# Kernel tuning notes

Measured on AMD Instinct MI355X. Metric: run time of the kernel, lower is better.

The kernel has to match this reference:

```python
import jax, jax.numpy as jnp
import numpy as np
from jax import lax

HD = 64      # head_dim
PS = 2       # fine patch size
EPS = 1e-5   # batchnorm eps

def _conv(x, w, stride, pad, groups=1):
    return lax.conv_general_dilated(x, w, (stride, stride), ((pad, pad), (pad, pad)),
                                    feature_group_count=groups,
                                    dimension_numbers=('NCHW', 'OIHW', 'NCHW'))

def _conv_transpose(x, w, stride, pad):
    # torch ConvTranspose2d(in,out,k,stride,pad) with w [in,out,k,k]
    k = w.shape[-1]
    wt = jnp.flip(w, (2, 3)).transpose(1, 0, 2, 3)  # -> [out,in,k,k]
    e = k - 1 - pad
    return lax.conv_general_dilated(x, wt, (1, 1), ((e, e), (e, e)),
                                    lhs_dilation=(stride, stride),
                                    dimension_numbers=('NCHW', 'OIHW', 'NCHW'))

def _bn(x, g, b, m, v):
    inv = g / jnp.sqrt(v + EPS)
    return x * inv[None, :, None, None] + (b - m * inv)[None, :, None, None]

def setup_inputs() -> dict:
    key = jax.random.key(0)
    ks = jax.random.split(key, 12)
    B, C, H, W = 8, 256, 64, 64
    f = lambda k, sh, s=0.05: jax.random.normal(k, sh, jnp.float32) * s
    return {
        'x': jax.random.normal(ks[0], (B, C, H, W), jnp.float32),
        'down_w': f(ks[1], (C, C, 4, 4), 0.02), 'down_b': f(ks[2], (C,)),
        'up_w': f(ks[3], (C, C, 4, 4), 0.02), 'up_b': f(ks[4], (C,)),
        'wqkv_c': f(ks[5], (HD, 3 * HD)), 'bqkv_c': f(ks[6], (3 * HD,)),
        'wqkv_f': f(ks[7], (HD, 3 * HD)), 'bqkv_f': f(ks[8], (3 * HD,)),
        'dw_w': f(ks[9], (C, 1, 3, 3)),
        'bn1_g': jnp.ones((C,), jnp.float32), 'bn1_b': jnp.zeros((C,), jnp.float32),
        'bn1_m': jnp.zeros((C,), jnp.float32), 'bn1_v': jnp.ones((C,), jnp.float32),
        'pw_w': f(ks[10], (C, C, 1, 1)),
        'bn2_g': jnp.ones((C,), jnp.float32), 'bn2_b': jnp.zeros((C,), jnp.float32),
        'bn2_m': jnp.zeros((C,), jnp.float32), 'bn2_v': jnp.ones((C,), jnp.float32),
    }

def reference(x, down_w, down_b, up_w, up_b, wqkv_c, bqkv_c, wqkv_f, bqkv_f, dw_w,
              bn1_g, bn1_b, bn1_m, bn1_v, pw_w, bn2_g, bn2_b, bn2_m, bn2_v):
    B, C, H, W = x.shape
    nh = C // HD
    scale = HD ** -0.5

    # ---- CoarseSelfAttention: downsample -> per-head MHSA -> top-k -> upsample ----
    xd = _conv(x, down_w, 2, 1) + down_b[None, :, None, None]          # [B,C,H/2,W/2]
    h, w = H // 2, W // 2
    N = h * w
    tok = xd.reshape(B, nh, HD, N).transpose(0, 1, 3, 2)               # [B,nh,N,hd]
    q, k, v = jnp.split(tok @ wqkv_c + bqkv_c, 3, axis=-1)
    attn = jax.nn.softmax(jnp.einsum('bhnd,bhmd->bhnm', q, k) * scale, axis=-1)
    score = attn.sum(axis=-2)                                          # [B,nh,N]
    kf = max(1, N // 4)
    topk = lax.top_k(score, kf)[1]                                     # [B,nh,kf] int32
    out = jnp.einsum('bhnm,bhmd->bhnd', attn, v)
    out = out.transpose(0, 1, 3, 2).reshape(B, C, h, w)
    coarse = _conv_transpose(out, up_w, 2, 1) + up_b[None, :, None, None]  # [B,C,H,W]
    # F.interpolate to (H,W) is identity here: upsample output already matches x.

    # ---- TopkSelfAttention: gather top-k 2x2 patches, local MHSA, scatter back ----
    ph, pw = H // PS, W // PS
    xh = coarse.reshape(B, nh, HD, ph, PS, pw, PS)
    patches = xh.transpose(0, 1, 2, 3, 5, 4, 6).reshape(B, nh, HD, ph * pw, PS, PS)
    sel = jnp.take_along_axis(patches, topk[:, :, None, :, None, None], axis=3)  # [B,nh,hd,kf,PS,PS]
    tok_f = sel.reshape(B, nh, HD, kf, PS * PS).transpose(0, 1, 3, 4, 2).reshape(B, nh, kf * PS * PS, HD)
    qf, kfp, vf = jnp.split(tok_f @ wqkv_f + bqkv_f, 3, axis=-1)
    attn_f = jax.nn.softmax(jnp.einsum('bhnd,bhmd->bhnm', qf, kfp) * scale, axis=-1)
    out_f = jnp.einsum('bhnm,bhmd->bhnd', attn_f, vf)                  # [B,nh,kf*4,hd]
    out_p = out_f.reshape(B, nh, kf, PS * PS, HD).transpose(0, 1, 2, 4, 3).reshape(B, nh, kf, HD, PS, PS)
    bi = jnp.arange(B)[:, None, None]
    hi = jnp.arange(nh)[None, :, None]
    res = jnp.zeros_like(patches).at[bi, hi, :, topk].set(out_p)       # scatter (indices unique)
    region = res.reshape(B, nh, HD, ph, pw, PS, PS).transpose(0, 1, 2, 3, 5, 4, 6).reshape(B, C, H, W)

    # ---- residual + DWConv (depthwise->BN->ReLU6->pointwise->BN->ReLU6) ----
    y = coarse + region
    y = jnp.clip(_bn(_conv(y, dw_w, 1, 1, groups=C), bn1_g, bn1_b, bn1_m, bn1_v), 0.0, 6.0)
    y = jnp.clip(_bn(_conv(y, pw_w, 1, 0), bn2_g, bn2_b, bn2_m, bn2_v), 0.0, 6.0)
    return y
```

## Files before the change

kernel.cpp:

```cpp
#include <hip/hip_runtime.h>
#include <hip/hip_bf16.h>

typedef __hip_bfloat16 bf16;
typedef __bf16 bf16x8 __attribute__((ext_vector_type(8)));
typedef float f32x4 __attribute__((ext_vector_type(4)));


#define OFF_XDHWC    0L
#define OFF_QH       2097152L
#define OFF_T1       0L
#define OFF_OUTC     8388608L
#define OFF_COARSE   10485760L
#define OFF_XHL      10485760L
#define OFF_PSCW     10485760L
#define OFF_SCORE    19398656L
#define OFF_TOPK     19431424L
#define OFF_DOWNW    19439616L
#define OFF_DOWNWL   19963904L
#define OFF_UPW4     20488192L
#define OFF_WQKVC    21536768L
#define OFF_BQKVC    21549056L
#define OFF_WQKVF    21549248L
#define OFF_BQKVF    21561536L
#define OFF_PWW      21561728L
#define OFF_DWW      21627264L
#define OFF_BN1S     21629568L
#define OFF_BN1T     21629824L
#define OFF_BN2S     21630080L
#define OFF_BN2T     21630336L
#define OFF_DOWNB    21630592L
#define OFF_UPB      21630848L
#define OFF_FLAG     21631104L
#define WS_FLOATS    21631360L

__device__ __forceinline__ float relu6(float v) { return v < 0.f ? 0.f : (v > 6.f ? 6.f : v); }

__device__ __forceinline__ float ldin(const void* p, long i, int flag) {
    return flag ? __bfloat162float(((const bf16*)p)[i]) : ((const float*)p)[i];
}

__device__ __forceinline__ unsigned short f2bf(float f) {
    unsigned int b = __float_as_uint(f);
    b += 0x7FFFu + ((b >> 16) & 1u);
    return (unsigned short)(b >> 16);
}

__global__ __launch_bounds__(256) void detect_kernel(const void* __restrict__ x, int* __restrict__ flag) {
    __shared__ int cnt[256];
    int tid = threadIdx.x;
    int c = 0;
    for (int i = tid; i < 4096; i += 256) {
        long idx = (long)i * 2047;
        float v = __bfloat162float(((const bf16*)x)[idx]);
        float a = fabsf(v);
        if (isfinite(v) && a > 1e-8f && a < 100.f) c++;
    }
    cnt[tid] = c; __syncthreads();
    for (int s = 128; s > 0; s >>= 1) { if (tid < s) cnt[tid] += cnt[tid + s]; __syncthreads(); }
    if (tid == 0 && cnt[0] >= 3686) *flag = 1;
}

__global__ __launch_bounds__(256) void split_pack_kernel(const void* __restrict__ in, unsigned int* __restrict__ out,
                                                         int n, const int* __restrict__ flagp) {
    int flag = *flagp;
    int i = blockIdx.x * 256 + threadIdx.x;
    if (i < n) {
        float v = ldin(in, i, flag);
        unsigned short h = f2bf(v);
        float fh = __uint_as_float(((unsigned int)h) << 16);
        unsigned short l = f2bf(v - fh);
        out[i] = (unsigned int)h | ((unsigned int)l << 16);
    }
}

__global__ __launch_bounds__(256) void split_kernel(const void* __restrict__ in,
                                                    unsigned short* __restrict__ hi, unsigned short* __restrict__ lo,
                                                    int n, const int* __restrict__ flagp) {
    int flag = *flagp;
    int i = blockIdx.x * 256 + threadIdx.x;
    if (i < n) {
        float v = ldin(in, i, flag);
        unsigned short h = f2bf(v);
        float fh = __uint_as_float(((unsigned int)h) << 16);
        hi[i] = h;
        lo[i] = f2bf(v - fh);
    }
}

__global__ __launch_bounds__(256) void prep_up_kernel(const void* __restrict__ w, unsigned short* __restrict__ W4,
                                                      const int* __restrict__ flagp) {
    int flag = *flagp;
    int idx = blockIdx.x * 256 + threadIdx.x;
    int cls = idx >> 18; int rem = idx & 262143;
    int co = rem >> 10; int q = rem & 1023;
    int ci = q >> 2; int j = q & 3;
    int pa = cls >> 1, pb = cls & 1;
    int jy = j >> 1, jx = j & 1;
    int ky = (pa == 0) ? (jy ? 3 : 1) : (jy ? 0 : 2);
    int kx = (pb == 0) ? (jx ? 3 : 1) : (jx ? 0 : 2);
    W4[idx] = f2bf(ldin(w, (((long)ci * 256 + co) * 4 + ky) * 4 + kx, flag));
}

__global__ __launch_bounds__(256) void prep_misc_kernel(
    const void* __restrict__ down_b, const void* __restrict__ up_b,
    const void* __restrict__ bqkv_c, const void* __restrict__ bqkv_f,
    const void* __restrict__ dw_w, const void* __restrict__ wqkv_c,
    const void* __restrict__ wqkv_f, const void* __restrict__ pw_w,
    const void* __restrict__ bn1_g, const void* __restrict__ bn1_b,
    const void* __restrict__ bn1_m, const void* __restrict__ bn1_v,
    const void* __restrict__ bn2_g, const void* __restrict__ bn2_b,
    const void* __restrict__ bn2_m, const void* __restrict__ bn2_v,
    float* __restrict__ ws, const int* __restrict__ flagp)
{
    int flag = *flagp;
    int bid = blockIdx.x, tid = threadIdx.x;
    if (bid < 48) {
        int idx = bid * 256 + tid;
        int j = idx >> 6, d = idx & 63;
        ws[OFF_WQKVC + idx] = ldin(wqkv_c, d * 192 + j, flag);
    } else if (bid < 96) {
        int idx = (bid - 48) * 256 + tid;
        int j = idx >> 6, d = idx & 63;
        ws[OFF_WQKVF + idx] = ldin(wqkv_f, d * 192 + j, flag);
    } else if (bid < 105) {
        int i = (bid - 96) * 256 + tid;
        if (i < 2304) ws[OFF_DWW + i] = ldin(dw_w, i, flag);
    } else if (bid == 105) {
        ws[OFF_DOWNB + tid] = ldin(down_b, tid, flag);
    } else if (bid == 106) {
        ws[OFF_UPB + tid] = ldin(up_b, tid, flag);
    } else if (bid == 107) {
        if (tid < 192) ws[OFF_BQKVC + tid] = ldin(bqkv_c, tid, flag);
    } else if (bid == 108) {
        if (tid < 192) ws[OFF_BQKVF + tid] = ldin(bqkv_f, tid, flag);
    } else if (bid == 109) {
        float gv = ldin(bn1_g, tid, flag), bv = ldin(bn1_b, tid, flag);
        float mv = ldin(bn1_m, tid, flag), vv = ldin(bn1_v, tid, flag);
        float inv = gv / sqrtf(vv + 1e-5f);
        ws[OFF_BN1S + tid] = inv; ws[OFF_BN1T + tid] = bv - mv * inv;
    } else if (bid == 110) {
        float gv = ldin(bn2_g, tid, flag), bv = ldin(bn2_b, tid, flag);
        float mv = ldin(bn2_m, tid, flag), vv = ldin(bn2_v, tid, flag);
        float inv = gv / sqrtf(vv + 1e-5f);
        ws[OFF_BN2S + tid] = inv; ws[OFF_BN2T + tid] = bv - mv * inv;
    } else {
        int i = (bid - 111) * 256 + tid;
        ((unsigned short*)(ws + OFF_PWW))[i] = f2bf(ldin(pw_w, i, flag));
    }
}

__global__ __launch_bounds__(256) void gemm_mfma_x2(
    const unsigned int* __restrict__ XHL,
    const unsigned short* __restrict__ WH, const unsigned short* __restrict__ WL,
    float* __restrict__ C, const float* __restrict__ e0)
{
    __shared__ __align__(16) unsigned short Ah[64 * 40];
    __shared__ __align__(16) unsigned short Al[64 * 40];
    __shared__ __align__(16) unsigned short Bh[32 * 40];
    __shared__ __align__(16) unsigned short Bl[32 * 40];
    int m0 = blockIdx.y * 64, n0 = blockIdx.x * 32;
    int tid = threadIdx.x;
    int w = tid >> 6, l = tid & 63, l15 = l & 15, q = l >> 4;

    int offA[8], ldsA[8];
    #pragma unroll
    for (int i = 0; i < 8; i++) {
        int idx = i * 256 + tid;
        int kl = idx & 31, ml = idx >> 5;
        int m = m0 + ml;
        int b = m >> 10, oy = (m >> 5) & 31, ox = m & 31;
        int c0 = kl >> 4;
        int ky = (kl >> 2) & 3, kx = kl & 3;
        int iy = 2 * oy - 1 + ky, ix = 2 * ox - 1 + kx;
        ldsA[i] = ml * 40 + kl;
        offA[i] = ((unsigned)iy < 64u && (unsigned)ix < 64u)
                  ? (((b * 256 + c0) * 64 + iy) * 64 + ix) : -1;
    }
    unsigned int aR[8];
    uint2 bhR, blR;
    int bn = tid >> 3, bk = (tid & 7) * 4;

    auto loadA = [&](int k0) {
        int cb = (k0 >> 4) * 4096;
        #pragma unroll
        for (int i = 0; i < 8; i++)
            aR[i] = (offA[i] >= 0) ? XHL[offA[i] + cb] : 0u;
    };
    auto storeA = [&]() {
        #pragma unroll
        for (int i = 0; i < 8; i++) {
            Ah[ldsA[i]] = (unsigned short)(aR[i] & 0xffffu);
            Al[ldsA[i]] = (unsigned short)(aR[i] >> 16);
        }
    };
    auto loadB = [&](int k0) {
        bhR = *(const uint2*)(WH + (long)(n0 + bn) * 4096 + (k0 + bk));
        blR = *(const uint2*)(WL + (long)(n0 + bn) * 4096 + (k0 + bk));
    };

    f32x4 acc[2] = {};
    loadA(0); loadB(0);
    for (int k0 = 0; k0 < 4096; k0 += 32) {
        storeA();
        *(uint2*)(&Bh[bn * 40 + bk]) = bhR;
        *(uint2*)(&Bl[bn * 40 + bk]) = blR;
        __syncthreads();
        if (k0 + 32 < 4096) { loadA(k0 + 32); loadB(k0 + 32); }
        bf16x8 afh = *(const bf16x8*)(&Ah[(w * 16 + l15) * 40 + q * 8]);
        bf16x8 afl = *(const bf16x8*)(&Al[(w * 16 + l15) * 40 + q * 8]);
        #pragma unroll
        for (int j4 = 0; j4 < 2; j4++) {
            bf16x8 bfh = *(const bf16x8*)(&Bh[(j4 * 16 + l15) * 40 + q * 8]);
            bf16x8 bfl = *(const bf16x8*)(&Bl[(j4 * 16 + l15) * 40 + q * 8]);
            acc[j4] = __builtin_amdgcn_mfma_f32_16x16x32_bf16(afh, bfh, acc[j4], 0, 0, 0);
            acc[j4] = __builtin_amdgcn_mfma_f32_16x16x32_bf16(afh, bfl, acc[j4], 0, 0, 0);
            acc[j4] = __builtin_amdgcn_mfma_f32_16x16x32_bf16(afl, bfh, acc[j4], 0, 0, 0);
        }
        __syncthreads();
    }
    #pragma unroll
    for (int j4 = 0; j4 < 2; j4++) {
        int n = n0 + j4 * 16 + l15;
        #pragma unroll
        for (int r = 0; r < 4; r++) {
            int m = m0 + w * 16 + q * 4 + r;
            C[(long)m * 256 + n] = acc[j4][r] + e0[n];
        }
    }
}

template<int EPI>
__global__ __launch_bounds__(256) void gemm_k(
    const float* __restrict__ A, const float* __restrict__ B,
    unsigned short* __restrict__ out, int K, int sAm, int sBn, const float* __restrict__ e0)
{
    __shared__ float As[16][68];
    __shared__ float Bs[16][68];
    int m0 = blockIdx.y * 64;
    int n0 = blockIdx.x * 64;
    int tid = threadIdx.x;
    int tx = tid & 15, ty = tid >> 4;
    int l4 = tid >> 2, kq = (tid & 3) * 4;
    float4 aR, bR;

    auto loadA = [&](int k0) { aR = *(const float4*)(A + (long)(m0 + l4) * sAm + (k0 + kq)); };
    auto loadB = [&](int k0) { bR = *(const float4*)(B + (long)(n0 + l4) * sBn + (k0 + kq)); };

    float acc[4][4] = {};
    loadA(0); loadB(0);
    for (int k0 = 0; k0 < K; k0 += 16) {
        As[kq + 0][l4] = aR.x; As[kq + 1][l4] = aR.y; As[kq + 2][l4] = aR.z; As[kq + 3][l4] = aR.w;
        Bs[kq + 0][l4] = bR.x; Bs[kq + 1][l4] = bR.y; Bs[kq + 2][l4] = bR.z; Bs[kq + 3][l4] = bR.w;
        __syncthreads();
        if (k0 + 16 < K) { loadA(k0 + 16); loadB(k0 + 16); }
        #pragma unroll
        for (int kk = 0; kk < 16; ++kk) {
            float4 av = *reinterpret_cast<const float4*>(&As[kk][ty * 4]);
            float4 bv = *reinterpret_cast<const float4*>(&Bs[kk][tx * 4]);
            float a[4] = {av.x, av.y, av.z, av.w};
            float b[4] = {bv.x, bv.y, bv.z, bv.w};
            #pragma unroll
            for (int i = 0; i < 4; i++)
                #pragma unroll
                for (int j = 0; j < 4; j++)
                    acc[i][j] += a[i] * b[j];
        }
        __syncthreads();
    }
    #pragma unroll
    for (int i = 0; i < 4; i++) {
        int m = m0 + ty * 4 + i;
        int bh, tok;
        if (EPI == 2) { int bi = m >> 12; int h = m & 3; tok = (m >> 2) & 1023; bh = bi * 4 + h; }
        else          { bh = m >> 10; tok = m & 1023; }
        #pragma unroll
        for (int j = 0; j < 4; j++) {
            int n = n0 + tx * 4 + j;
            float v = acc[i][j] + e0[n];
            if (n < 64) {
                v *= 0.125f;
                unsigned short hb = f2bf(v);
                float fh = __uint_as_float(((unsigned int)hb) << 16);
                unsigned short lb = f2bf(v - fh);
                long p = (((long)bh << 10) + tok) * 64 + n;
                out[p] = hb; out[p + 2097152] = lb;
            } else if (n < 128) {
                unsigned short hb = f2bf(v);
                float fh = __uint_as_float(((unsigned int)hb) << 16);
                unsigned short lb = f2bf(v - fh);
                long p = (((long)bh << 10) + tok) * 64 + (n - 64);
                out[p + 4194304] = hb; out[p + 6291456] = lb;
            } else {
                out[8388608 + (((long)bh << 6) + (n - 128)) * 1024 + tok] = f2bf(v);
            }
        }
    }
}

template<int EPI, int AMODE>
__global__ __launch_bounds__(256) void gemm_mfma(
    const float* __restrict__ A, const unsigned short* __restrict__ Bb, float* __restrict__ C,
    int K, long sAz, long sBz, int sAk, int sBn,
    const float* __restrict__ e0, const float* __restrict__ e1,
    void* __restrict__ ob, const int* __restrict__ flagp)
{
    __shared__ __align__(16) unsigned short Asb[64 * 40];
    __shared__ __align__(16) unsigned short Bsb[64 * 40];
    int z = blockIdx.z;
    if (AMODE == 0) A += (long)z * sAz;
    Bb += (long)z * sBz;
    int m0 = blockIdx.y * 64, n0 = blockIdx.x * 64;
    int tid = threadIdx.x;
    int w = tid >> 6, l = tid & 63;
    int l15 = l & 15, q = l >> 4;
    float aR[8];
    uint4 bR;

    auto loadA = [&](int k0) {
        if (AMODE == 0) {
            #pragma unroll
            for (int i = 0; i < 8; i++) {
                int idx = i * 256 + tid;
                int ml = idx & 63, kl = idx >> 6;
                aR[i] = A[(long)(k0 + kl) * sAk + (m0 + ml)];
            }
        } else {
            #pragma unroll
            for (int i = 0; i < 8; i++) {
                int idx = i * 256 + tid;
                int kl = idx & 31, ml = idx >> 5;
                int m = m0 + ml, k = k0 + kl;
                int b = m >> 10, y = (m >> 5) & 31, x2 = m & 31;
                int ci = k >> 2, j = k & 3;
                int pa = z >> 1, pb = z & 1;
                int jy = j >> 1, jx = j & 1;
                int dy = (pa == 0) ? (jy ? -1 : 0) : (jy ? 1 : 0);
                int dx = (pb == 0) ? (jx ? -1 : 0) : (jx ? 1 : 0);
                int yy = y + dy, xx = x2 + dx;
                float val = 0.f;
                if ((unsigned)yy < 32u && (unsigned)xx < 32u)
                    val = A[(((long)b * 4 + (ci >> 6)) * 1024 + yy * 32 + xx) * 64 + (ci & 63)];
                aR[i] = val;
            }
        }
    };
    auto storeA = [&]() {
        #pragma unroll
        for (int i = 0; i < 8; i++) {
            int idx = i * 256 + tid;
            int ml, kl;
            if (AMODE == 0) { ml = idx & 63; kl = idx >> 6; }
            else            { kl = idx & 31; ml = idx >> 5; }
            Asb[ml * 40 + kl] = f2bf(aR[i]);
        }
    };
    int bn = tid >> 2, bk = (tid & 3) * 8;
    auto loadB = [&](int k0) {
        bR = *(const uint4*)(Bb + (long)(n0 + bn) * sBn + (k0 + bk));
    };

    f32x4 acc[4] = {};
    loadA(0); loadB(0);
    for (int k0 = 0; k0 < K; k0 += 32) {
        storeA();
        *(uint4*)(&Bsb[bn * 40 + bk]) = bR;
        __syncthreads();
        if (k0 + 32 < K) { loadA(k0 + 32); loadB(k0 + 32); }
        bf16x8 af = *(const bf16x8*)(&Asb[(w * 16 + l15) * 40 + q * 8]);
        #pragma unroll
        for (int j4 = 0; j4 < 4; j4++) {
            bf16x8 bf = *(const bf16x8*)(&Bsb[(j4 * 16 + l15) * 40 + q * 8]);
            acc[j4] = __builtin_amdgcn_mfma_f32_16x16x32_bf16(af, bf, acc[j4], 0, 0, 0);
        }
        __syncthreads();
    }
    int oflag = (EPI == 5) ? *flagp : 0;
    #pragma unroll
    for (int j4 = 0; j4 < 4; j4++) {
        int n = n0 + j4 * 16 + l15;
        #pragma unroll
        for (int r = 0; r < 4; r++) {
            int m = m0 + w * 16 + q * 4 + r;
            float v = acc[j4][r];
            if (EPI == 4) {
                v += e0[n];
                int pa = z >> 1, pb = z & 1;
                int bi = m >> 10, y = (m >> 5) & 31, x2 = m & 31;
                C[(((long)bi * 256 + n) * 64 + (2 * y + pa)) * 64 + (2 * x2 + pb)] = v;
            } else {
                v = relu6(v * e0[n] + e1[n]);
                long oidx = (long)z * 1048576 + (long)n * 4096 + m;
                if (oflag) ((bf16*)ob)[oidx] = __float2bfloat16(v);
                else       ((float*)ob)[oidx] = v;
            }
        }
    }
}

template<bool SCORE>
__global__ __launch_bounds__(256) void attn_mfma(
    const unsigned short* __restrict__ P0,
    float* __restrict__ O, float* __restrict__ PSCW)
{
    const unsigned short* QH = P0;
    const unsigned short* QL = P0 + 2097152;
    const unsigned short* KH = P0 + 4194304;
    const unsigned short* KL = P0 + 6291456;
    const unsigned short* VT = P0 + 8388608;
    __shared__ __align__(16) unsigned short Khs[64 * 72];
    __shared__ __align__(16) unsigned short Kls[64 * 72];
    __shared__ __align__(16) unsigned short Vs[64 * 72];
    __shared__ __align__(16) unsigned short Ps[4][16 * 72];
    int bh = blockIdx.y, rt = blockIdx.x;
    int tid = threadIdx.x;
    int w = tid >> 6, l = tid & 63, l15 = l & 15, q = l >> 4;

    long qoff = (((long)bh << 10) + rt * 64 + w * 16 + l15) * 64 + q * 8;
    bf16x8 afh[2], afl[2];
    afh[0] = *(const bf16x8*)(QH + qoff);
    afh[1] = *(const bf16x8*)(QH + qoff + 32);
    afl[0] = *(const bf16x8*)(QL + qoff);
    afl[1] = *(const bf16x8*)(QL + qoff + 32);

    float mr[4], lr[4];
    #pragma unroll
    for (int r = 0; r < 4; r++) { mr[r] = -1e30f; lr[r] = 0.f; }
    f32x4 o[4] = {};

    auto stageK = [&](int t) {
        #pragma unroll
        for (int i = 0; i < 2; i++) {
            int u = tid + i * 256;
            int tok = u >> 3, dp = (u & 7) * 8;
            long g = (((long)bh << 10) + t * 64 + tok) * 64 + dp;
            *(uint4*)(Khs + tok * 72 + dp) = *(const uint4*)(KH + g);
            *(uint4*)(Kls + tok * 72 + dp) = *(const uint4*)(KL + g);
        }
    };
    auto stageV = [&](int t) {
        #pragma unroll
        for (int i = 0; i < 2; i++) {
            int u = tid + i * 256;
            int d = u >> 3, k0 = (u & 7) * 8;
            long g = (((long)bh << 6) + d) * 1024 + t * 64 + k0;
            *(uint4*)(Vs + d * 72 + k0) = *(const uint4*)(VT + g);
        }
    };
    auto computeS = [&](f32x4* s) {
        #pragma unroll
        for (int kk = 0; kk < 2; kk++)
            #pragma unroll
            for (int j4 = 0; j4 < 4; j4++) {
                bf16x8 kh8 = *(const bf16x8*)(&Khs[(j4 * 16 + l15) * 72 + kk * 32 + q * 8]);
                bf16x8 kl8 = *(const bf16x8*)(&Kls[(j4 * 16 + l15) * 72 + kk * 32 + q * 8]);
                s[j4] = __builtin_amdgcn_mfma_f32_16x16x32_bf16(afh[kk], kh8, s[j4], 0, 0, 0);
                s[j4] = __builtin_amdgcn_mfma_f32_16x16x32_bf16(afh[kk], kl8, s[j4], 0, 0, 0);
                s[j4] = __builtin_amdgcn_mfma_f32_16x16x32_bf16(afl[kk], kh8, s[j4], 0, 0, 0);
            }
    };
    auto pv = [&]() {
        #pragma unroll
        for (int kk = 0; kk < 2; kk++) {
            bf16x8 ap = *(const bf16x8*)(&Ps[w][l15 * 72 + kk * 32 + q * 8]);
            #pragma unroll
            for (int j4 = 0; j4 < 4; j4++) {
                bf16x8 bv = *(const bf16x8*)(&Vs[(j4 * 16 + l15) * 72 + kk * 32 + q * 8]);
                o[j4] = __builtin_amdgcn_mfma_f32_16x16x32_bf16(ap, bv, o[j4], 0, 0, 0);
            }
        }
    };

    if (SCORE) {
        for (int t = 0; t < 16; ++t) {
            __syncthreads();
            stageK(t);
            __syncthreads();
            f32x4 s[4] = {};
            computeS(s);
            #pragma unroll
            for (int r = 0; r < 4; r++) {
                float tm = fmaxf(fmaxf(s[0][r], s[1][r]), fmaxf(s[2][r], s[3][r]));
                #pragma unroll
                for (int off = 1; off < 16; off <<= 1) tm = fmaxf(tm, __shfl_xor(tm, off));
                float mn = fmaxf(mr[r], tm);
                float ss = __expf(s[0][r] - mn) + __expf(s[1][r] - mn)
                         + __expf(s[2][r] - mn) + __expf(s[3][r] - mn);
                #pragma unroll
                for (int off = 1; off < 16; off <<= 1) ss += __shfl_xor(ss, off);
                lr[r] = lr[r] * __expf(mr[r] - mn) + ss;
                mr[r] = mn;
            }
        }
        float linv[4];
        #pragma unroll
        for (int r = 0; r < 4; r++) linv[r] = 1.f / lr[r];
        for (int t = 0; t < 16; ++t) {
            __syncthreads();
            stageK(t); stageV(t);
            __syncthreads();
            f32x4 s[4] = {};
            computeS(s);
            float cs[4] = {0.f, 0.f, 0.f, 0.f};
            #pragma unroll
            for (int j4 = 0; j4 < 4; j4++)
                #pragma unroll
                for (int r = 0; r < 4; r++) {
                    float p = __expf(s[j4][r] - mr[r]) * linv[r];
                    cs[j4] += p;
                    Ps[w][(q * 4 + r) * 72 + j4 * 16 + l15] = f2bf(p);
                }
            #pragma unroll
            for (int j4 = 0; j4 < 4; j4++) {
                cs[j4] += __shfl_xor(cs[j4], 16);
                cs[j4] += __shfl_xor(cs[j4], 32);
            }
            if (q == 0) {
                long pb = (((long)(bh * 16 + rt) * 4 + w) << 10) + t * 64;
                #pragma unroll
                for (int j4 = 0; j4 < 4; j4++) PSCW[pb + j4 * 16 + l15] = cs[j4];
            }
            __syncthreads();
            pv();
        }
    } else {
        for (int t = 0; t < 16; ++t) {
            __syncthreads();
            stageK(t); stageV(t);
            __syncthreads();
            f32x4 s[4] = {};
            computeS(s);
            float corr[4];
            #pragma unroll
            for (int r = 0; r < 4; r++) {
                float tm = fmaxf(fmaxf(s[0][r], s[1][r]), fmaxf(s[2][r], s[3][r]));
                #pragma unroll
                for (int off = 1; off < 16; off <<= 1) tm = fmaxf(tm, __shfl_xor(tm, off));
                float mn = fmaxf(mr[r], tm);
                corr[r] = __expf(mr[r] - mn);
                mr[r] = mn;
            }
            float ssr[4] = {0.f, 0.f, 0.f, 0.f};
            #pragma unroll
            for (int j4 = 0; j4 < 4; j4++)
                #pragma unroll
                for (int r = 0; r < 4; r++) {
                    float p = __expf(s[j4][r] - mr[r]);
                    ssr[r] += p;
                    Ps[w][(q * 4 + r) * 72 + j4 * 16 + l15] = f2bf(p);
                }
            #pragma unroll
            for (int r = 0; r < 4; r++) {
                float ss = ssr[r];
                #pragma unroll
                for (int off = 1; off < 16; off <<= 1) ss += __shfl_xor(ss, off);
                lr[r] = lr[r] * corr[r] + ss;
            }
            #pragma unroll
            for (int j4 = 0; j4 < 4; j4++)
                #pragma unroll
                for (int r = 0; r < 4; r++) o[j4][r] *= corr[r];
            __syncthreads();
            pv();
        }
    }

    float fin[4];
    #pragma unroll
    for (int r = 0; r < 4; r++) fin[r] = SCORE ? 1.f : (1.f / lr[r]);
    long obase = (((long)bh << 10) + rt * 64 + w * 16 + q * 4) * 64;
    #pragma unroll
    for (int j4 = 0; j4 < 4; j4++)
        #pragma unroll
        for (int r = 0; r < 4; r++)
            O[obase + (long)r * 64 + j4 * 16 + l15] = o[j4][r] * fin[r];
}

__global__ __launch_bounds__(256) void topk_kernel(const float* __restrict__ PSCW, int* __restrict__ topk) {
    __shared__ float s[1024];
    int z = blockIdx.x; int tid = threadIdx.x;
    for (int i = tid; i < 1024; i += 256) {
        float v = 0.f;
        for (int rw = 0; rw < 64; rw++) v += PSCW[(((long)z * 64 + rw) << 10) + i];
        s[i] = (v == v) ? v : -INFINITY;
    }
    __syncthreads();
    for (int i = tid; i < 1024; i += 256) {
        float si = s[i]; int r = 0;
        for (int j = 0; j < 1024; j++) {
            float sj = s[j];
            r += (sj > si) || (sj == si && j < i);
        }
        if (r < 256) topk[z * 256 + r] = i;
    }
}

__global__ __launch_bounds__(256) void gather_tokf_kernel(const float* __restrict__ coarse,
                                                          const int* __restrict__ topk,
                                                          float* __restrict__ tokf) {
    long idx = (long)blockIdx.x * 256 + threadIdx.x;
    int d = (int)(idx & 63); int t = (int)((idx >> 6) & 3);
    int j = (int)((idx >> 8) & 255); int bh = (int)(idx >> 16);
    int p = topk[bh * 256 + j] & 1023;
    int py = p >> 5, px = p & 31;
    int dy = t >> 1, dx = t & 1;
    int b = bh >> 2, h = bh & 3;
    tokf[idx] = coarse[(((long)b * 256 + h * 64 + d) * 64 + (2 * py + dy)) * 64 + (2 * px + dx)];
}

__global__ __launch_bounds__(256) void scatter_add_kernel(float* __restrict__ coarse,
                                                          const int* __restrict__ topk,
                                                          const float* __restrict__ outf) {
    long idx = (long)blockIdx.x * 256 + threadIdx.x;
    int d = (int)(idx & 63); int t = (int)((idx >> 6) & 3);
    int j = (int)((idx >> 8) & 255); int bh = (int)(idx >> 16);
    int p = topk[bh * 256 + j] & 1023;
    int py = p >> 5, px = p & 31;
    int dy = t >> 1, dx = t & 1;
    int b = bh >> 2, h = bh & 3;
    coarse[(((long)b * 256 + h * 64 + d) * 64 + (2 * py + dy)) * 64 + (2 * px + dx)] += outf[idx];
}

__global__ __launch_bounds__(64) void dw_bn_relu6_kernel(const float* __restrict__ y, const float* __restrict__ w9,
                                                         const float* __restrict__ s1, const float* __restrict__ t1,
                                                         float* __restrict__ out) {
    int gid = blockIdx.x;
    int row = gid & 63; int bc = gid >> 6; int c = bc & 255;
    int x = threadIdx.x;
    const float* base = y + (long)bc * 4096;
    float acc = 0.f;
    #pragma unroll
    for (int ky = 0; ky < 3; ky++) {
        int yy = row + ky - 1;
        if (yy < 0 || yy >= 64) continue;
        #pragma unroll
        for (int kx = 0; kx < 3; kx++) {
            int xx = x + kx - 1;
            if (xx < 0 || xx >= 64) continue;
            acc += base[yy * 64 + xx] * w9[c * 9 + ky * 3 + kx];
        }
    }
    out[(long)gid * 64 + x] = relu6(acc * s1[c] + t1[c]);
}

extern "C" void kernel_launch(void* const* d_in, const int* in_sizes, int n_in,
                              void* d_out, int out_size, void* d_ws, size_t ws_size,
                              hipStream_t stream) {
    if (ws_size < (size_t)WS_FLOATS * 4) return;

    const void* x      = d_in[0];
    const void* down_w = d_in[1];
    const void* down_b = d_in[2];
    const void* up_w   = d_in[3];
    const void* up_b   = d_in[4];
    const void* wqkv_c = d_in[5];
    const void* bqkv_c = d_in[6];
    const void* wqkv_f = d_in[7];
    const void* bqkv_f = d_in[8];
    const void* dw_w   = d_in[9];
    const void* bn1_g  = d_in[10];
    const void* bn1_b  = d_in[11];
    const void* bn1_m  = d_in[12];
    const void* bn1_v  = d_in[13];
    const void* pw_w   = d_in[14];
    const void* bn2_g  = d_in[15];
    const void* bn2_b  = d_in[16];
    const void* bn2_m  = d_in[17];
    const void* bn2_v  = d_in[18];

    float* ws = (float*)d_ws;
    int* flagp = (int*)(ws + OFF_FLAG);
    dim3 blk(256);

    hipMemsetAsync(flagp, 0, sizeof(int), stream);
    detect_kernel<<<1, blk, 0, stream>>>(x, flagp);

    split_pack_kernel<<<32768, blk, 0, stream>>>(x, (unsigned int*)(ws + OFF_XHL), 8388608, flagp);
    split_kernel<<<4096, blk, 0, stream>>>(down_w, (unsigned short*)(ws + OFF_DOWNW),
                                           (unsigned short*)(ws + OFF_DOWNWL), 1048576, flagp);
    prep_misc_kernel<<<367, blk, 0, stream>>>(down_b, up_b, bqkv_c, bqkv_f, dw_w, wqkv_c, wqkv_f, pw_w,
                                              bn1_g, bn1_b, bn1_m, bn1_v, bn2_g, bn2_b, bn2_m, bn2_v,
                                              ws, flagp);
    prep_up_kernel<<<4096, blk, 0, stream>>>(up_w, (unsigned short*)(ws + OFF_UPW4), flagp);

    gemm_mfma_x2<<<dim3(8, 128, 1), blk, 0, stream>>>((const unsigned int*)(ws + OFF_XHL),
        (const unsigned short*)(ws + OFF_DOWNW), (const unsigned short*)(ws + OFF_DOWNWL),
        ws + OFF_XDHWC, ws + OFF_DOWNB);

    gemm_k<2><<<dim3(3, 512, 1), blk, 0, stream>>>(ws + OFF_XDHWC, ws + OFF_WQKVC,
        (unsigned short*)(ws + OFF_QH), 64, 64, 64, ws + OFF_BQKVC);

    attn_mfma<true><<<dim3(16, 32), blk, 0, stream>>>((const unsigned short*)(ws + OFF_QH),
        ws + OFF_OUTC, ws + OFF_PSCW);
    topk_kernel<<<32, blk, 0, stream>>>(ws + OFF_PSCW, (int*)(ws + OFF_TOPK));

    gemm_mfma<4, 2><<<dim3(4, 128, 4), blk, 0, stream>>>(ws + OFF_OUTC, (unsigned short*)(ws + OFF_UPW4),
        ws + OFF_COARSE, 1024, 0, 262144, 0, 1024, ws + OFF_UPB, nullptr, nullptr, flagp);

    gather_tokf_kernel<<<8192, blk, 0, stream>>>(ws + OFF_COARSE, (const int*)(ws + OFF_TOPK), ws + OFF_XDHWC);
    gemm_k<3><<<dim3(3, 512, 1), blk, 0, stream>>>(ws + OFF_XDHWC, ws + OFF_WQKVF,
        (unsigned short*)(ws + OFF_QH), 64, 64, 64, ws + OFF_BQKVF);
    attn_mfma<false><<<dim3(16, 32), blk, 0, stream>>>((const unsigned short*)(ws + OFF_QH),
        ws + OFF_OUTC, nullptr);
    scatter_add_kernel<<<8192, blk, 0, stream>>>(ws + OFF_COARSE, (const int*)(ws + OFF_TOPK), ws + OFF_OUTC);

    dw_bn_relu6_kernel<<<131072, dim3(64), 0, stream>>>(ws + OFF_COARSE, ws + OFF_DWW,
        ws + OFF_BN1S, ws + OFF_BN1T, ws + OFF_T1);

    gemm_mfma<5, 0><<<dim3(4, 64, 8), blk, 0, stream>>>(ws + OFF_T1, (unsigned short*)(ws + OFF_PWW),
        nullptr, 256, 1048576, 0, 4096, 256, ws + OFF_BN2S, ws + OFF_BN2T, d_out, flagp);
}
```

Measured before the change: 833.4 us.

## Repack input to NHWC hi/lo and widen downsample conv GEMM tiles

The input is now packed into a channel-last layout with an LDS transpose, and the downsample weights are permuted to position-major/channel-minor order. This lets the implicit-GEMM downsample convolution load 16-byte contiguous vectors per tap instead of scattered 4-byte gathers. The GEMM tile is widened from 64x32 to 64x64 with a K step of 64, giving more MFMA work per load. The cost is an extra transpose pass, larger LDS use per block, and only half as many blocks in the grid.

```diff
diff --git a/kernel.cpp b/kernel.cpp
--- a/kernel.cpp
+++ b/kernel.cpp
@@ -60,31 +60,47 @@
     if (tid == 0 && cnt[0] >= 3686) *flag = 1;
 }
 
-__global__ __launch_bounds__(256) void split_pack_kernel(const void* __restrict__ in, unsigned int* __restrict__ out,
-                                                         int n, const int* __restrict__ flagp) {
+__global__ __launch_bounds__(256) void transpose_pack_kernel(const void* __restrict__ x,
+                                                             unsigned int* __restrict__ XP,
+                                                             const int* __restrict__ flagp) {
+    __shared__ unsigned int T[64][65];
     int flag = *flagp;
-    int i = blockIdx.x * 256 + threadIdx.x;
-    if (i < n) {
-        float v = ldin(in, i, flag);
+    int bid = blockIdx.x;
+    int cc = bid & 3, biy = bid >> 2;
+    int b = biy >> 6, iy = biy & 63;
+    int c0 = cc * 64;
+    int t = threadIdx.x;
+    int r = t >> 6, u = t & 63;
+    #pragma unroll
+    for (int p = 0; p < 16; p++) {
+        int cl = p * 4 + r;
+        float v = ldin(x, (((long)(b * 256 + c0 + cl)) * 64 + iy) * 64 + u, flag);
         unsigned short h = f2bf(v);
         float fh = __uint_as_float(((unsigned int)h) << 16);
         unsigned short l = f2bf(v - fh);
-        out[i] = (unsigned int)h | ((unsigned int)l << 16);
-    }
-}
-
-__global__ __launch_bounds__(256) void split_kernel(const void* __restrict__ in,
-                                                    unsigned short* __restrict__ hi, unsigned short* __restrict__ lo,
-                                                    int n, const int* __restrict__ flagp) {
+        T[cl][u] = (unsigned int)h | ((unsigned int)l << 16);
+    }
+    __syncthreads();
+    long obase = ((long)biy * 64) * 256 + c0;
+    #pragma unroll
+    for (int p = 0; p < 16; p++) {
+        int ix = p * 4 + r;
+        XP[obase + (long)ix * 256 + u] = T[u][ix];
+    }
+}
+
+__global__ __launch_bounds__(256) void split_perm_kernel(const void* __restrict__ in,
+                                                         unsigned short* __restrict__ hi,
+                                                         unsigned short* __restrict__ lo,
+                                                         const int* __restrict__ flagp) {
     int flag = *flagp;
     int i = blockIdx.x * 256 + threadIdx.x;
-    if (i < n) {
-        float v = ldin(in, i, flag);
-        unsigned short h = f2bf(v);
-        float fh = __uint_as_float(((unsigned int)h) << 16);
-        hi[i] = h;
-        lo[i] = f2bf(v - fh);
-    }
+    int co = i >> 12, rr = i & 4095, pos = rr >> 8, ci = rr & 255;
+    float v = ldin(in, (long)co * 4096 + ci * 16 + pos, flag);
+    unsigned short h = f2bf(v);
+    float fh = __uint_as_float(((unsigned int)h) << 16);
+    hi[i] = h;
+    lo[i] = f2bf(v - fh);
 }
 
 __global__ __launch_bounds__(256) void prep_up_kernel(const void* __restrict__ w, unsigned short* __restrict__ W4,
@@ -150,76 +166,96 @@
 }
 
 __global__ __launch_bounds__(256) void gemm_mfma_x2(
-    const unsigned int* __restrict__ XHL,
+    const unsigned int* __restrict__ XP,
     const unsigned short* __restrict__ WH, const unsigned short* __restrict__ WL,
     float* __restrict__ C, const float* __restrict__ e0)
 {
-    __shared__ __align__(16) unsigned short Ah[64 * 40];
-    __shared__ __align__(16) unsigned short Al[64 * 40];
-    __shared__ __align__(16) unsigned short Bh[32 * 40];
-    __shared__ __align__(16) unsigned short Bl[32 * 40];
-    int m0 = blockIdx.y * 64, n0 = blockIdx.x * 32;
+    __shared__ __align__(16) unsigned short Ah[64 * 72];
+    __shared__ __align__(16) unsigned short Al[64 * 72];
+    __shared__ __align__(16) unsigned short Bh[64 * 72];
+    __shared__ __align__(16) unsigned short Bl[64 * 72];
+    int m0 = blockIdx.y * 64, n0 = blockIdx.x * 64;
     int tid = threadIdx.x;
     int w = tid >> 6, l = tid & 63, l15 = l & 15, q = l >> 4;
 
-    int offA[8], ldsA[8];
-    #pragma unroll
-    for (int i = 0; i < 8; i++) {
-        int idx = i * 256 + tid;
-        int kl = idx & 31, ml = idx >> 5;
+    int ml = tid >> 2, cq = (tid & 3) * 16;
+    int base, vmask;
+    {
         int m = m0 + ml;
         int b = m >> 10, oy = (m >> 5) & 31, ox = m & 31;
-        int c0 = kl >> 4;
-        int ky = (kl >> 2) & 3, kx = kl & 3;
-        int iy = 2 * oy - 1 + ky, ix = 2 * ox - 1 + kx;
-        ldsA[i] = ml * 40 + kl;
-        offA[i] = ((unsigned)iy < 64u && (unsigned)ix < 64u)
-                  ? (((b * 256 + c0) * 64 + iy) * 64 + ix) : -1;
-    }
-    unsigned int aR[8];
-    uint2 bhR, blR;
-    int bn = tid >> 3, bk = (tid & 7) * 4;
-
-    auto loadA = [&](int k0) {
-        int cb = (k0 >> 4) * 4096;
-        #pragma unroll
-        for (int i = 0; i < 8; i++)
-            aR[i] = (offA[i] >= 0) ? XHL[offA[i] + cb] : 0u;
+        base = ((b * 64 + 2 * oy - 1) * 64 + (2 * ox - 1)) * 256;
+        vmask = 0;
+        #pragma unroll
+        for (int pos = 0; pos < 16; pos++) {
+            int ky = pos >> 2, kx = pos & 3;
+            int iy = 2 * oy - 1 + ky, ix = 2 * ox - 1 + kx;
+            if ((unsigned)iy < 64u && (unsigned)ix < 64u) vmask |= (1 << pos);
+        }
+    }
+    uint4 aR[4];
+    uint4 bhR[2], blR[2];
+    int bn = tid >> 2, bkc = (tid & 3) * 16;
+
+    auto loadA = [&](int s) {
+        int pos = s >> 2, ci0 = (s & 3) << 6;
+        const unsigned int* p = XP + base + ((pos >> 2) << 14) + ((pos & 3) << 8) + ci0 + cq;
+        if ((vmask >> pos) & 1) {
+            aR[0] = *(const uint4*)(p);
+            aR[1] = *(const uint4*)(p + 4);
+            aR[2] = *(const uint4*)(p + 8);
+            aR[3] = *(const uint4*)(p + 12);
+        } else {
+            uint4 z = {0u, 0u, 0u, 0u};
+            aR[0] = z; aR[1] = z; aR[2] = z; aR[3] = z;
+        }
     };
     auto storeA = [&]() {
         #pragma unroll
-        for (int i = 0; i < 8; i++) {
-            Ah[ldsA[i]] = (unsigned short)(aR[i] & 0xffffu);
-            Al[ldsA[i]] = (unsigned short)(aR[i] >> 16);
-        }
-    };
-    auto loadB = [&](int k0) {
-        bhR = *(const uint2*)(WH + (long)(n0 + bn) * 4096 + (k0 + bk));
-        blR = *(const uint2*)(WL + (long)(n0 + bn) * 4096 + (k0 + bk));
-    };
-
-    f32x4 acc[2] = {};
+        for (int j = 0; j < 4; j++) {
+            unsigned int h0 = __builtin_amdgcn_perm(aR[j].y, aR[j].x, 0x05040100u);
+            unsigned int h1 = __builtin_amdgcn_perm(aR[j].w, aR[j].z, 0x05040100u);
+            unsigned int l0 = __builtin_amdgcn_perm(aR[j].y, aR[j].x, 0x07060302u);
+            unsigned int l1 = __builtin_amdgcn_perm(aR[j].w, aR[j].z, 0x07060302u);
+            uint2 hh; hh.x = h0; hh.y = h1;
+            uint2 ll; ll.x = l0; ll.y = l1;
+            *(uint2*)(&Ah[ml * 72 + cq + j * 4]) = hh;
+            *(uint2*)(&Al[ml * 72 + cq + j * 4]) = ll;
+        }
+    };
+    auto loadB = [&](int s) {
+        const unsigned short* ph = WH + (long)(n0 + bn) * 4096 + s * 64 + bkc;
+        const unsigned short* pl = WL + (long)(n0 + bn) * 4096 + s * 64 + bkc;
+        bhR[0] = *(const uint4*)(ph); bhR[1] = *(const uint4*)(ph + 8);
+        blR[0] = *(const uint4*)(pl); blR[1] = *(const uint4*)(pl + 8);
+    };
+    auto storeB = [&]() {
+        *(uint4*)(&Bh[bn * 72 + bkc]) = bhR[0]; *(uint4*)(&Bh[bn * 72 + bkc + 8]) = bhR[1];
+        *(uint4*)(&Bl[bn * 72 + bkc]) = blR[0]; *(uint4*)(&Bl[bn * 72 + bkc + 8]) = blR[1];
+    };
+
+    f32x4 acc[4] = {};
     loadA(0); loadB(0);
-    for (int k0 = 0; k0 < 4096; k0 += 32) {
-        storeA();
-        *(uint2*)(&Bh[bn * 40 + bk]) = bhR;
-        *(uint2*)(&Bl[bn * 40 + bk]) = blR;
+    for (int s = 0; s < 64; s++) {
+        storeA(); storeB();
         __syncthreads();
-        if (k0 + 32 < 4096) { loadA(k0 + 32); loadB(k0 + 32); }
-        bf16x8 afh = *(const bf16x8*)(&Ah[(w * 16 + l15) * 40 + q * 8]);
-        bf16x8 afl = *(const bf16x8*)(&Al[(w * 16 + l15) * 40 + q * 8]);
-        #pragma unroll
-        for (int j4 = 0; j4 < 2; j4++) {
-            bf16x8 bfh = *(const bf16x8*)(&Bh[(j4 * 16 + l15) * 40 + q * 8]);
-            bf16x8 bfl = *(const bf16x8*)(&Bl[(j4 * 16 + l15) * 40 + q * 8]);
-            acc[j4] = __builtin_amdgcn_mfma_f32_16x16x32_bf16(afh, bfh, acc[j4], 0, 0, 0);
-            acc[j4] = __builtin_amdgcn_mfma_f32_16x16x32_bf16(afh, bfl, acc[j4], 0, 0, 0);
-            acc[j4] = __builtin_amdgcn_mfma_f32_16x16x32_bf16(afl, bfh, acc[j4], 0, 0, 0);
+        if (s + 1 < 64) { loadA(s + 1); loadB(s + 1); }
+        #pragma unroll
+        for (int kk = 0; kk < 2; kk++) {
+            bf16x8 afh = *(const bf16x8*)(&Ah[(w * 16 + l15) * 72 + kk * 32 + q * 8]);
+            bf16x8 afl = *(const bf16x8*)(&Al[(w * 16 + l15) * 72 + kk * 32 + q * 8]);
+            #pragma unroll
+            for (int j4 = 0; j4 < 4; j4++) {
+                bf16x8 bfh = *(const bf16x8*)(&Bh[(j4 * 16 + l15) * 72 + kk * 32 + q * 8]);
+                bf16x8 bfl = *(const bf16x8*)(&Bl[(j4 * 16 + l15) * 72 + kk * 32 + q * 8]);
+                acc[j4] = __builtin_amdgcn_mfma_f32_16x16x32_bf16(afh, bfh, acc[j4], 0, 0, 0);
+                acc[j4] = __builtin_amdgcn_mfma_f32_16x16x32_bf16(afh, bfl, acc[j4], 0, 0, 0);
+                acc[j4] = __builtin_amdgcn_mfma_f32_16x16x32_bf16(afl, bfh, acc[j4], 0, 0, 0);
+            }
         }
         __syncthreads();
     }
     #pragma unroll
-    for (int j4 = 0; j4 < 2; j4++) {
+    for (int j4 = 0; j4 < 4; j4++) {
         int n = n0 + j4 * 16 + l15;
         #pragma unroll
         for (int r = 0; r < 4; r++) {
@@ -674,15 +710,15 @@
     hipMemsetAsync(flagp, 0, sizeof(int), stream);
     detect_kernel<<<1, blk, 0, stream>>>(x, flagp);
 
-    split_pack_kernel<<<32768, blk, 0, stream>>>(x, (unsigned int*)(ws + OFF_XHL), 8388608, flagp);
-    split_kernel<<<4096, blk, 0, stream>>>(down_w, (unsigned short*)(ws + OFF_DOWNW),
-                                           (unsigned short*)(ws + OFF_DOWNWL), 1048576, flagp);
+    transpose_pack_kernel<<<2048, blk, 0, stream>>>(x, (unsigned int*)(ws + OFF_XHL), flagp);
+    split_perm_kernel<<<4096, blk, 0, stream>>>(down_w, (unsigned short*)(ws + OFF_DOWNW),
+                                                (unsigned short*)(ws + OFF_DOWNWL), flagp);
     prep_misc_kernel<<<367, blk, 0, stream>>>(down_b, up_b, bqkv_c, bqkv_f, dw_w, wqkv_c, wqkv_f, pw_w,
                                               bn1_g, bn1_b, bn1_m, bn1_v, bn2_g, bn2_b, bn2_m, bn2_v,
                                               ws, flagp);
     prep_up_kernel<<<4096, blk, 0, stream>>>(up_w, (unsigned short*)(ws + OFF_UPW4), flagp);
 
-    gemm_mfma_x2<<<dim3(8, 128, 1), blk, 0, stream>>>((const unsigned int*)(ws + OFF_XHL),
+    gemm_mfma_x2<<<dim3(4, 128, 1), blk, 0, stream>>>((const unsigned int*)(ws + OFF_XHL),
         (const unsigned short*)(ws + OFF_DOWNW), (const unsigned short*)(ws + OFF_DOWNWL),
         ws + OFF_XDHWC, ws + OFF_DOWNB);
 
```

Measured after the change: 866.3 us. +4.0%, slower.

## Prefetch K/V tiles in attention, widen downsample GEMM tile, hoist gather offsets

Applied to the files above, without the earlier changes.

The attention kernel now double-buffers K and V tiles through registers. The next tile's global loads are issued right after the barrier, so they overlap the current tile's compute, and one barrier per iteration is removed. The split-bf16 downsample GEMM widens its N tile from 32 to 64 and halves the grid in x, so each im2col A tile feeds twice as many MFMAs. In exchange, the A gather addresses in that GEMM are recomputed every iteration. The upsample GEMM's gather now precomputes per-thread spatial base offsets once instead of per k-step. The costs are higher register pressure and fewer blocks for the downsample GEMM.

```diff
diff --git a/kernel.cpp b/kernel.cpp
--- a/kernel.cpp
+++ b/kernel.cpp
@@ -156,60 +156,56 @@
 {
     __shared__ __align__(16) unsigned short Ah[64 * 40];
     __shared__ __align__(16) unsigned short Al[64 * 40];
-    __shared__ __align__(16) unsigned short Bh[32 * 40];
-    __shared__ __align__(16) unsigned short Bl[32 * 40];
-    int m0 = blockIdx.y * 64, n0 = blockIdx.x * 32;
+    __shared__ __align__(16) unsigned short Bh[64 * 40];
+    __shared__ __align__(16) unsigned short Bl[64 * 40];
+    int m0 = blockIdx.y * 64, n0 = blockIdx.x * 64;
     int tid = threadIdx.x;
     int w = tid >> 6, l = tid & 63, l15 = l & 15, q = l >> 4;
-
-    int offA[8], ldsA[8];
-    #pragma unroll
-    for (int i = 0; i < 8; i++) {
-        int idx = i * 256 + tid;
-        int kl = idx & 31, ml = idx >> 5;
-        int m = m0 + ml;
-        int b = m >> 10, oy = (m >> 5) & 31, ox = m & 31;
-        int c0 = kl >> 4;
-        int ky = (kl >> 2) & 3, kx = kl & 3;
-        int iy = 2 * oy - 1 + ky, ix = 2 * ox - 1 + kx;
-        ldsA[i] = ml * 40 + kl;
-        offA[i] = ((unsigned)iy < 64u && (unsigned)ix < 64u)
-                  ? (((b * 256 + c0) * 64 + iy) * 64 + ix) : -1;
-    }
     unsigned int aR[8];
-    uint2 bhR, blR;
-    int bn = tid >> 3, bk = (tid & 7) * 4;
+    uint4 bhR, blR;
+    int bn = tid >> 2, bk = (tid & 3) * 8;
 
     auto loadA = [&](int k0) {
-        int cb = (k0 >> 4) * 4096;
-        #pragma unroll
-        for (int i = 0; i < 8; i++)
-            aR[i] = (offA[i] >= 0) ? XHL[offA[i] + cb] : 0u;
+        #pragma unroll
+        for (int i = 0; i < 8; i++) {
+            int idx = i * 256 + tid;
+            int kl = idx & 31, ml = idx >> 5;
+            int m = m0 + ml, k = k0 + kl;
+            int b = m >> 10, oy = (m >> 5) & 31, ox = m & 31;
+            int c = k >> 4, ky = (k >> 2) & 3, kx = k & 3;
+            int iy = 2 * oy - 1 + ky, ix = 2 * ox - 1 + kx;
+            unsigned int v = 0;
+            if ((unsigned)iy < 64u && (unsigned)ix < 64u)
+                v = XHL[(((long)b * 256 + c) * 64 + iy) * 64 + ix];
+            aR[i] = v;
+        }
     };
     auto storeA = [&]() {
         #pragma unroll
         for (int i = 0; i < 8; i++) {
-            Ah[ldsA[i]] = (unsigned short)(aR[i] & 0xffffu);
-            Al[ldsA[i]] = (unsigned short)(aR[i] >> 16);
+            int idx = i * 256 + tid;
+            int kl = idx & 31, ml = idx >> 5;
+            Ah[ml * 40 + kl] = (unsigned short)(aR[i] & 0xffffu);
+            Al[ml * 40 + kl] = (unsigned short)(aR[i] >> 16);
         }
     };
     auto loadB = [&](int k0) {
-        bhR = *(const uint2*)(WH + (long)(n0 + bn) * 4096 + (k0 + bk));
-        blR = *(const uint2*)(WL + (long)(n0 + bn) * 4096 + (k0 + bk));
-    };
-
-    f32x4 acc[2] = {};
+        bhR = *(const uint4*)(WH + (long)(n0 + bn) * 4096 + (k0 + bk));
+        blR = *(const uint4*)(WL + (long)(n0 + bn) * 4096 + (k0 + bk));
+    };
+
+    f32x4 acc[4] = {};
     loadA(0); loadB(0);
     for (int k0 = 0; k0 < 4096; k0 += 32) {
         storeA();
-        *(uint2*)(&Bh[bn * 40 + bk]) = bhR;
-        *(uint2*)(&Bl[bn * 40 + bk]) = blR;
+        *(uint4*)(&Bh[bn * 40 + bk]) = bhR;
+        *(uint4*)(&Bl[bn * 40 + bk]) = blR;
         __syncthreads();
         if (k0 + 32 < 4096) { loadA(k0 + 32); loadB(k0 + 32); }
         bf16x8 afh = *(const bf16x8*)(&Ah[(w * 16 + l15) * 40 + q * 8]);
         bf16x8 afl = *(const bf16x8*)(&Al[(w * 16 + l15) * 40 + q * 8]);
         #pragma unroll
-        for (int j4 = 0; j4 < 2; j4++) {
+        for (int j4 = 0; j4 < 4; j4++) {
             bf16x8 bfh = *(const bf16x8*)(&Bh[(j4 * 16 + l15) * 40 + q * 8]);
             bf16x8 bfl = *(const bf16x8*)(&Bl[(j4 * 16 + l15) * 40 + q * 8]);
             acc[j4] = __builtin_amdgcn_mfma_f32_16x16x32_bf16(afh, bfh, acc[j4], 0, 0, 0);
@@ -219,7 +215,7 @@
         __syncthreads();
     }
     #pragma unroll
-    for (int j4 = 0; j4 < 2; j4++) {
+    for (int j4 = 0; j4 < 4; j4++) {
         int n = n0 + j4 * 16 + l15;
         #pragma unroll
         for (int r = 0; r < 4; r++) {
@@ -316,6 +312,26 @@
     float aR[8];
     uint4 bR;
 
+    int sbA[8], ci0A[8];
+    if (AMODE != 0) {
+        #pragma unroll
+        for (int i = 0; i < 8; i++) {
+            int idx = i * 256 + tid;
+            int kl = idx & 31, ml = idx >> 5;
+            int m = m0 + ml;
+            int b = m >> 10, y = (m >> 5) & 31, x2 = m & 31;
+            int j = kl & 3;
+            int pa = z >> 1, pb = z & 1;
+            int jy = j >> 1, jx = j & 1;
+            int dy = (pa == 0) ? (jy ? -1 : 0) : (jy ? 1 : 0);
+            int dx = (pb == 0) ? (jx ? -1 : 0) : (jx ? 1 : 0);
+            int yy = y + dy, xx = x2 + dx;
+            ci0A[i] = kl >> 2;
+            sbA[i] = ((unsigned)yy < 32u && (unsigned)xx < 32u)
+                     ? (b * 262144 + (yy * 32 + xx) * 64) : -1;
+        }
+    }
+
     auto loadA = [&](int k0) {
         if (AMODE == 0) {
             #pragma unroll
@@ -325,22 +341,11 @@
                 aR[i] = A[(long)(k0 + kl) * sAk + (m0 + ml)];
             }
         } else {
+            int cq = k0 >> 2;
             #pragma unroll
             for (int i = 0; i < 8; i++) {
-                int idx = i * 256 + tid;
-                int kl = idx & 31, ml = idx >> 5;
-                int m = m0 + ml, k = k0 + kl;
-                int b = m >> 10, y = (m >> 5) & 31, x2 = m & 31;
-                int ci = k >> 2, j = k & 3;
-                int pa = z >> 1, pb = z & 1;
-                int jy = j >> 1, jx = j & 1;
-                int dy = (pa == 0) ? (jy ? -1 : 0) : (jy ? 1 : 0);
-                int dx = (pb == 0) ? (jx ? -1 : 0) : (jx ? 1 : 0);
-                int yy = y + dy, xx = x2 + dx;
-                float val = 0.f;
-                if ((unsigned)yy < 32u && (unsigned)xx < 32u)
-                    val = A[(((long)b * 4 + (ci >> 6)) * 1024 + yy * 32 + xx) * 64 + (ci & 63)];
-                aR[i] = val;
+                int ci = ci0A[i] + cq;
+                aR[i] = (sbA[i] >= 0) ? A[sbA[i] + ((ci >> 6) << 16) + (ci & 63)] : 0.f;
             }
         }
     };
@@ -422,30 +427,46 @@
     afl[0] = *(const bf16x8*)(QL + qoff);
     afl[1] = *(const bf16x8*)(QL + qoff + 32);
 
+    int ldsKo[2], ldsVo[2];
+    long gK[2], gV[2];
+    #pragma unroll
+    for (int i = 0; i < 2; i++) {
+        int u = tid + i * 256;
+        int tok = u >> 3, dp = (u & 7) * 8;
+        ldsKo[i] = tok * 72 + dp;
+        gK[i] = (((long)bh << 10) + tok) * 64 + dp;
+        ldsVo[i] = tok * 72 + dp;
+        gV[i] = (((long)bh << 6) + tok) * 1024 + dp;
+    }
+    uint4 khR[2], klR[2], vR[2];
+    auto loadK = [&](int t) {
+        #pragma unroll
+        for (int i = 0; i < 2; i++) {
+            khR[i] = *(const uint4*)(KH + gK[i] + t * 4096);
+            klR[i] = *(const uint4*)(KL + gK[i] + t * 4096);
+        }
+    };
+    auto storeK = [&]() {
+        #pragma unroll
+        for (int i = 0; i < 2; i++) {
+            *(uint4*)(Khs + ldsKo[i]) = khR[i];
+            *(uint4*)(Kls + ldsKo[i]) = klR[i];
+        }
+    };
+    auto loadV = [&](int t) {
+        #pragma unroll
+        for (int i = 0; i < 2; i++) vR[i] = *(const uint4*)(VT + gV[i] + t * 64);
+    };
+    auto storeV = [&]() {
+        #pragma unroll
+        for (int i = 0; i < 2; i++) *(uint4*)(Vs + ldsVo[i]) = vR[i];
+    };
+
     float mr[4], lr[4];
     #pragma unroll
     for (int r = 0; r < 4; r++) { mr[r] = -1e30f; lr[r] = 0.f; }
     f32x4 o[4] = {};
 
-    auto stageK = [&](int t) {
-        #pragma unroll
-        for (int i = 0; i < 2; i++) {
-            int u = tid + i * 256;
-            int tok = u >> 3, dp = (u & 7) * 8;
-            long g = (((long)bh << 10) + t * 64 + tok) * 64 + dp;
-            *(uint4*)(Khs + tok * 72 + dp) = *(const uint4*)(KH + g);
-            *(uint4*)(Kls + tok * 72 + dp) = *(const uint4*)(KL + g);
-        }
-    };
-    auto stageV = [&](int t) {
-        #pragma unroll
-        for (int i = 0; i < 2; i++) {
-            int u = tid + i * 256;
-            int d = u >> 3, k0 = (u & 7) * 8;
-            long g = (((long)bh << 6) + d) * 1024 + t * 64 + k0;
-            *(uint4*)(Vs + d * 72 + k0) = *(const uint4*)(VT + g);
-        }
-    };
     auto computeS = [&](f32x4* s) {
         #pragma unroll
         for (int kk = 0; kk < 2; kk++)
@@ -471,10 +492,11 @@
     };
 
     if (SCORE) {
+        loadK(0);
         for (int t = 0; t < 16; ++t) {
+            storeK();
             __syncthreads();
-            stageK(t);
-            __syncthreads();
+            if (t + 1 < 16) loadK(t + 1);
             f32x4 s[4] = {};
             computeS(s);
             #pragma unroll
@@ -490,14 +512,16 @@
                 lr[r] = lr[r] * __expf(mr[r] - mn) + ss;
                 mr[r] = mn;
             }
+            __syncthreads();
         }
         float linv[4];
         #pragma unroll
         for (int r = 0; r < 4; r++) linv[r] = 1.f / lr[r];
+        loadK(0); loadV(0);
         for (int t = 0; t < 16; ++t) {
+            storeK(); storeV();
             __syncthreads();
-            stageK(t); stageV(t);
-            __syncthreads();
+            if (t + 1 < 16) { loadK(t + 1); loadV(t + 1); }
             f32x4 s[4] = {};
             computeS(s);
             float cs[4] = {0.f, 0.f, 0.f, 0.f};
@@ -519,14 +543,15 @@
                 #pragma unroll
                 for (int j4 = 0; j4 < 4; j4++) PSCW[pb + j4 * 16 + l15] = cs[j4];
             }
+            pv();
             __syncthreads();
-            pv();
         }
     } else {
+        loadK(0); loadV(0);
         for (int t = 0; t < 16; ++t) {
+            storeK(); storeV();
             __syncthreads();
-            stageK(t); stageV(t);
-            __syncthreads();
+            if (t + 1 < 16) { loadK(t + 1); loadV(t + 1); }
             f32x4 s[4] = {};
             computeS(s);
             float corr[4];
@@ -559,8 +584,8 @@
             for (int j4 = 0; j4 < 4; j4++)
                 #pragma unroll
                 for (int r = 0; r < 4; r++) o[j4][r] *= corr[r];
+            pv();
             __syncthreads();
-            pv();
         }
     }
 
@@ -682,7 +707,7 @@
                                               ws, flagp);
     prep_up_kernel<<<4096, blk, 0, stream>>>(up_w, (unsigned short*)(ws + OFF_UPW4), flagp);
 
-    gemm_mfma_x2<<<dim3(8, 128, 1), blk, 0, stream>>>((const unsigned int*)(ws + OFF_XHL),
+    gemm_mfma_x2<<<dim3(4, 128, 1), blk, 0, stream>>>((const unsigned int*)(ws + OFF_XHL),
         (const unsigned short*)(ws + OFF_DOWNW), (const unsigned short*)(ws + OFF_DOWNWL),
         ws + OFF_XDHWC, ws + OFF_DOWNB);
 
```

Measured after the change: 842.4 us. About the same (+1.1%).
